# Kernel optimization log

Hardware: AMD Instinct MI355X
Metric: run time of the kernel (lower is better)

Reference implementation:

```python
import jax, jax.numpy as jnp
import numpy as np

N = 50000      # nodes
E = 800000     # edges (avg degree 16)
HID = 64       # hidden_dim
NH = 4         # heads
HC = HID // NH # channels per head = 16
EMB = 8        # emb_dim
EDIM = 6       # edge_dim
SDIM = 6       # state_dim
FEAT = 7       # raw node feature width
NSENS = 3


def setup_inputs() -> dict:
    key = jax.random.key(0)
    k = jax.random.split(key, 32)
    s = 0.1
    p = {}
    p['x'] = jax.random.normal(k[0], (N, FEAT), jnp.float32)
    p['node_type'] = jax.random.randint(k[1], (N,), 0, 2)
    p['sensor_id'] = jax.random.randint(k[2], (N,), 0, NSENS + 1)
    p['edge_index'] = jax.random.randint(k[3], (2, E), 0, N)
    p['edge_attr'] = jax.random.normal(k[4], (E, EDIM), jnp.float32)
    p['hidden_state'] = jnp.zeros((N, HID), jnp.float32)
    # embeddings
    p['type_emb'] = jax.random.normal(k[5], (2, EMB)) * s
    p['sensor_emb'] = jax.random.normal(k[6], (NSENS + 1, EMB)) * s
    # encoder MLP
    p['enc_w1'] = jax.random.normal(k[7], (FEAT + 2 * EMB, HID)) * s
    p['enc_b1'] = jnp.zeros((HID,))
    p['enc_w2'] = jax.random.normal(k[8], (HID, HID)) * s
    p['enc_b2'] = jnp.zeros((HID,))
    # GATv2 layer 1 (lin_l, lin_r with bias; lin_edge no bias; att [NH,HC]; out bias)
    p['g1_wl'] = jax.random.normal(k[9], (HID, HID)) * s
    p['g1_bl'] = jnp.zeros((HID,))
    p['g1_wr'] = jax.random.normal(k[10], (HID, HID)) * s
    p['g1_br'] = jnp.zeros((HID,))
    p['g1_we'] = jax.random.normal(k[11], (EDIM, HID)) * s
    p['g1_att'] = jax.random.normal(k[12], (NH, HC)) * s
    p['g1_bias'] = jnp.zeros((HID,))
    # GATv2 layer 2
    p['g2_wl'] = jax.random.normal(k[13], (HID, HID)) * s
    p['g2_bl'] = jnp.zeros((HID,))
    p['g2_wr'] = jax.random.normal(k[14], (HID, HID)) * s
    p['g2_br'] = jnp.zeros((HID,))
    p['g2_we'] = jax.random.normal(k[15], (EDIM, HID)) * s
    p['g2_att'] = jax.random.normal(k[16], (NH, HC)) * s
    p['g2_bias'] = jnp.zeros((HID,))
    # GRUCell (torch layout transposed: [in, 3*hid], gate order r,z,n)
    p['gru_wih'] = jax.random.normal(k[17], (HID, 3 * HID)) * s
    p['gru_bih'] = jnp.zeros((3 * HID,))
    p['gru_whh'] = jax.random.normal(k[18], (HID, 3 * HID)) * s
    p['gru_bhh'] = jnp.zeros((3 * HID,))
    # decoder MLP
    p['dec_w1'] = jax.random.normal(k[19], (HID, HID)) * s
    p['dec_b1'] = jnp.zeros((HID,))
    p['dec_w2'] = jax.random.normal(k[20], (HID, SDIM + 1)) * s
    p['dec_b2'] = jnp.zeros((SDIM + 1,))
    return p


def _gatv2(h, src, dst, edge_attr, wl, bl, wr, br, we, att, bias):
    # PyG GATv2Conv, concat=True, negative_slope=0.2, edge_dim features
    xl = (h @ wl + bl).reshape(-1, NH, HC)  # source transform [N,H,C]
    xr = (h @ wr + br).reshape(-1, NH, HC)  # target transform [N,H,C]
    xe = (edge_attr @ we).reshape(-1, NH, HC)  # edge transform [E,H,C]
    m = jax.nn.leaky_relu(xl[src] + xr[dst] + xe, 0.2)  # [E,H,C]
    logits = jnp.einsum('ehc,hc->eh', m, att)  # [E,H]
    # scatter-softmax over incoming edges of each destination node
    mx = jax.ops.segment_max(logits, dst, num_segments=N)
    ex = jnp.exp(logits - mx[dst])
    den = jax.ops.segment_sum(ex, dst, num_segments=N)
    alpha = ex / (den[dst] + 1e-16)  # [E,H]
    out = jax.ops.segment_sum(xl[src] * alpha[:, :, None], dst, num_segments=N)
    return out.reshape(-1, NH * HC) + bias, alpha


def reference(x, node_type, sensor_id, edge_index, edge_attr, hidden_state,
              type_emb, sensor_emb, enc_w1, enc_b1, enc_w2, enc_b2,
              g1_wl, g1_bl, g1_wr, g1_br, g1_we, g1_att, g1_bias,
              g2_wl, g2_bl, g2_wr, g2_br, g2_we, g2_att, g2_bias,
              gru_wih, gru_bih, gru_whh, gru_bhh,
              dec_w1, dec_b1, dec_w2, dec_b2):
    src, dst = edge_index[0], edge_index[1]
    h = jnp.concatenate([x, type_emb[node_type], sensor_emb[sensor_id]], axis=-1)
    h = jax.nn.relu(h @ enc_w1 + enc_b1) @ enc_w2 + enc_b2
    h, alpha1 = _gatv2(h, src, dst, edge_attr, g1_wl, g1_bl, g1_wr, g1_br, g1_we, g1_att, g1_bias)
    h = jax.nn.relu(h)
    h, alpha2 = _gatv2(h, src, dst, edge_attr, g2_wl, g2_bl, g2_wr, g2_br, g2_we, g2_att, g2_bias)
    # GRUCell (torch gate order: r, z, n)
    gi = h @ gru_wih + gru_bih
    gh = hidden_state @ gru_whh + gru_bhh
    r = jax.nn.sigmoid(gi[:, :HID] + gh[:, :HID])
    z = jax.nn.sigmoid(gi[:, HID:2 * HID] + gh[:, HID:2 * HID])
    n = jnp.tanh(gi[:, 2 * HID:] + r * gh[:, 2 * HID:])
    new_hidden = (1.0 - z) * n + z * hidden_state
    out = jax.nn.relu(new_hidden @ dec_w1 + dec_b1) @ dec_w2 + dec_b2
    return out, new_hidden, alpha1, alpha2
```

## Files before the change

kernel.cpp:

```cpp
#include <hip/hip_runtime.h>
#include <hip/hip_bf16.h>

static constexpr int N_ = 50000;
static constexpr int E_ = 800000;
static constexpr int CAP = 128;


#define GEMM_FMA_BLOCK(AV, W0, W1, ROW)                                              \
      acc[ROW][0]=fmaf(AV,W0.x,acc[ROW][0]); acc[ROW][1]=fmaf(AV,W0.y,acc[ROW][1]);  \
      acc[ROW][2]=fmaf(AV,W0.z,acc[ROW][2]); acc[ROW][3]=fmaf(AV,W0.w,acc[ROW][3]);  \
      acc[ROW][4]=fmaf(AV,W1.x,acc[ROW][4]); acc[ROW][5]=fmaf(AV,W1.y,acc[ROW][5]);  \
      acc[ROW][6]=fmaf(AV,W1.z,acc[ROW][6]); acc[ROW][7]=fmaf(AV,W1.w,acc[ROW][7]);

#define GEMM_KLOOP(KQc)                                                              \
  _Pragma("unroll 1")                                                                \
  for (int kg = 0; kg < (KQc); ++kg) {                                               \
    float4 a0 = At4[kg * 129 + rowb];                                                \
    float4 a1 = At4[kg * 129 + rowb + 32];                                           \
    float4 a2 = At4[kg * 129 + rowb + 64];                                           \
    float4 a3 = At4[kg * 129 + rowb + 96];                                           \
    _Pragma("unroll")                                                                \
    for (int t = 0; t < 4; ++t) {                                                    \
      float4 w0 = *(const float4*)(Wt + (kg * 4 + t) * 64 + j0);                     \
      float4 w1 = *(const float4*)(Wt + (kg * 4 + t) * 64 + j0 + 4);                 \
      float av0 = t==0?a0.x:t==1?a0.y:t==2?a0.z:a0.w;                                \
      float av1 = t==0?a1.x:t==1?a1.y:t==2?a1.z:a1.w;                                \
      float av2 = t==0?a2.x:t==1?a2.y:t==2?a2.z:a2.w;                                \
      float av3 = t==0?a3.x:t==1?a3.y:t==2?a3.z:a3.w;                                \
      GEMM_FMA_BLOCK(av0, w0, w1, 0)                                                 \
      GEMM_FMA_BLOCK(av1, w0, w1, 1)                                                 \
      GEMM_FMA_BLOCK(av2, w0, w1, 2)                                                 \
      GEMM_FMA_BLOCK(av3, w0, w1, 3)                                                 \
    }                                                                                \
  }

#define ACC_INIT(BPTR)                                                               \
  {                                                                                  \
    float4 b0v = *(const float4*)((BPTR) + j0);                                      \
    float4 b1v = *(const float4*)((BPTR) + j0 + 4);                                  \
    _Pragma("unroll")                                                                \
    for (int i = 0; i < 4; ++i) {                                                    \
      acc[i][0]=b0v.x; acc[i][1]=b0v.y; acc[i][2]=b0v.z; acc[i][3]=b0v.w;            \
      acc[i][4]=b1v.x; acc[i][5]=b1v.y; acc[i][6]=b1v.z; acc[i][7]=b1v.w;            \
    }                                                                                \
  }

#define STAGE_W(WPTR, LDW, KPADc, KREAL)                                             \
  for (int idx = tid; idx < (KPADc) * 16; idx += 256) {                              \
    int k = idx >> 4, jq = idx & 15;                                                 \
    float4 v = (k < (KREAL)) ? *(const float4*)((WPTR) + (size_t)k * (LDW) + jq * 4) \
                             : make_float4(0.f, 0.f, 0.f, 0.f);                      \
    *(float4*)(Wt + k * 64 + jq * 4) = v;                                            \
  }

#define STAGE_A(APTR, LDA, KQc)                                                      \
  for (int idx = tid; idx < 128 * (KQc); idx += 256) {                               \
    int r = idx / (KQc), kq = idx - r * (KQc);                                       \
    int node = nb + r;                                                               \
    float4 v = (node < N_) ? *(const float4*)((APTR) + (size_t)node * (LDA) + kq * 4)\
                           : make_float4(0.f, 0.f, 0.f, 0.f);                        \
    At4[kq * 129 + r] = v;                                                           \
  }

#define STORE_C(CPTR, LDC, RELUc, ACCc)                                              \
  _Pragma("unroll")                                                                  \
  for (int i = 0; i < 4; ++i) {                                                      \
    int node = nb + rowb + 32 * i;                                                   \
    if (node < N_) {                                                                 \
      float* cp = (CPTR) + (size_t)node * (LDC) + j0;                                \
      float o0=acc[i][0],o1=acc[i][1],o2=acc[i][2],o3=acc[i][3];                     \
      float o4=acc[i][4],o5=acc[i][5],o6=acc[i][6],o7=acc[i][7];                     \
      if (RELUc) { o0=fmaxf(o0,0.f);o1=fmaxf(o1,0.f);o2=fmaxf(o2,0.f);o3=fmaxf(o3,0.f); \
                   o4=fmaxf(o4,0.f);o5=fmaxf(o5,0.f);o6=fmaxf(o6,0.f);o7=fmaxf(o7,0.f); } \
      if (ACCc) { float4 c0=*(const float4*)cp; float4 c1=*(const float4*)(cp+4);    \
                  o0+=c0.x;o1+=c0.y;o2+=c0.z;o3+=c0.w;o4+=c1.x;o5+=c1.y;o6+=c1.z;o7+=c1.w; } \
      *(float4*)cp = make_float4(o0,o1,o2,o3);                                       \
      *(float4*)(cp+4) = make_float4(o4,o5,o6,o7);                                   \
    }                                                                                \
  }

__global__ void k_hist(const int* __restrict__ ei, int* __restrict__ deg) {
  int e = blockIdx.x * blockDim.x + threadIdx.x;
  if (e < E_) atomicAdd(&deg[ei[E_ + e]], 1);
}

__global__ __launch_bounds__(1024) void k_scan_blk(const int* __restrict__ deg,
                                                   int* __restrict__ off,
                                                   int* __restrict__ bsum) {
  __shared__ int sm[1024];
  int t = threadIdx.x;
  int i = blockIdx.x * 1024 + t;
  int v = (i < N_) ? deg[i] : 0;
  sm[t] = v;
  __syncthreads();
  for (int s = 1; s < 1024; s <<= 1) {
    int u = (t >= s) ? sm[t - s] : 0;
    __syncthreads();
    sm[t] += u;
    __syncthreads();
  }
  if (i < N_) off[i] = sm[t] - v;
  if (t == 1023) bsum[blockIdx.x] = sm[t];
}

__global__ void k_scan_top(int* __restrict__ bsum, int nb) {
  int t = threadIdx.x;
  int v = (t < nb) ? bsum[t] : 0;
  int orig = v;
  for (int s = 1; s < 64; s <<= 1) {
    int u = __shfl_up(v, s);
    if (t >= s) v += u;
  }
  if (t < nb) bsum[t] = v - orig;
}

__global__ void k_scan_add(int* __restrict__ off, const int* __restrict__ bsum,
                           int* __restrict__ cur) {
  int i = blockIdx.x * blockDim.x + threadIdx.x;
  if (i < N_) {
    int o = off[i] + bsum[i >> 10];
    off[i] = o;
    cur[i] = o;
  }
  if (i == 0) off[N_] = E_;
}

__global__ void k_scatter(const int* __restrict__ ei, int* __restrict__ cursor,
                          int2* __restrict__ csr_es) {
  int e = blockIdx.x * blockDim.x + threadIdx.x;
  if (e < E_) {
    int s = ei[e];
    int d = ei[E_ + e];
    int p = atomicAdd(&cursor[d], 1);
    csr_es[p] = make_int2(e, s);
  }
}

__device__ __forceinline__ float encval(int c, int node, int nt, int sd,
                                        const float* __restrict__ x,
                                        const float* __restrict__ temb,
                                        const float* __restrict__ semb) {
  if (c < 7) return x[node * 7 + c];
  if (c < 15) return temb[nt * 8 + c - 7];
  if (c < 23) return semb[sd * 8 + c - 15];
  return 0.f;
}

__global__ __launch_bounds__(256, 3) void k_enc(
    const float* __restrict__ x, const int* __restrict__ ntype, const int* __restrict__ sid,
    const float* __restrict__ temb, const float* __restrict__ semb,
    const float* __restrict__ w1, const float* __restrict__ b1,
    const float* __restrict__ w2, const float* __restrict__ b2,
    float* __restrict__ hout) {
  __shared__ float4 At4[16 * 129];
  __shared__ float Wt[64 * 64];
  int tid = threadIdx.x;
  int nb = blockIdx.x * 128;
  for (int idx = tid; idx < 128 * 6; idx += 256) {
    int r = idx / 6, kq = idx - r * 6;
    int node = nb + r;
    float v0 = 0.f, v1 = 0.f, v2 = 0.f, v3 = 0.f;
    if (node < N_) {
      int nt = ntype[node], sd = sid[node];
      int c = kq * 4;
      v0 = encval(c, node, nt, sd, x, temb, semb);
      v1 = encval(c + 1, node, nt, sd, x, temb, semb);
      v2 = encval(c + 2, node, nt, sd, x, temb, semb);
      v3 = encval(c + 3, node, nt, sd, x, temb, semb);
    }
    At4[kq * 129 + r] = make_float4(v0, v1, v2, v3);
  }
  STAGE_W(w1, 64, 24, 23)
  __syncthreads();
  int col = tid & 7, rowb = tid >> 3;
  int j0 = col * 8;
  float acc[4][8];
  ACC_INIT(b1)
  GEMM_KLOOP(6)
  __syncthreads();
#pragma unroll
  for (int i = 0; i < 4; ++i) {
    int rl = rowb + 32 * i;
    At4[(col * 2) * 129 + rl] =
        make_float4(fmaxf(acc[i][0], 0.f), fmaxf(acc[i][1], 0.f),
                    fmaxf(acc[i][2], 0.f), fmaxf(acc[i][3], 0.f));
    At4[(col * 2 + 1) * 129 + rl] =
        make_float4(fmaxf(acc[i][4], 0.f), fmaxf(acc[i][5], 0.f),
                    fmaxf(acc[i][6], 0.f), fmaxf(acc[i][7], 0.f));
  }
  STAGE_W(w2, 64, 64, 64)
  __syncthreads();
  ACC_INIT(b2)
  GEMM_KLOOP(16)
  STORE_C(hout, 64, false, false)
}

__global__ __launch_bounds__(256, 3) void k_gemm2(
    const float* __restrict__ A,
    const float* __restrict__ Wl, const float* __restrict__ bl,
    const float* __restrict__ Wr, const float* __restrict__ br,
    float* __restrict__ Cl, float* __restrict__ Cr) {
  __shared__ float4 At4[16 * 129];
  __shared__ float Wt[64 * 64];
  int tid = threadIdx.x;
  int nb = blockIdx.x * 128;
  const float* W = blockIdx.y ? Wr : Wl;
  const float* b = blockIdx.y ? br : bl;
  float* C       = blockIdx.y ? Cr : Cl;
  STAGE_A(A, 64, 16)
  STAGE_W(W, 64, 64, 64)
  __syncthreads();
  int col = tid & 7, rowb = tid >> 3;
  int j0 = col * 8;
  float acc[4][8];
  ACC_INIT(b)
  GEMM_KLOOP(16)
  STORE_C(C, 64, false, false)
}

__global__ __launch_bounds__(256, 3) void k_gru(
    const float* __restrict__ hA, const float* __restrict__ hs,
    const float* __restrict__ wih, const float* __restrict__ bih,
    const float* __restrict__ whh, const float* __restrict__ bhh,
    float* __restrict__ outnh) {
  __shared__ float4 At4[16 * 129];
  __shared__ float Wt[64 * 64];
  int tid = threadIdx.x;
  int nb = blockIdx.x * 128;
  int col = tid & 7, rowb = tid >> 3;
  int j0 = col * 8;
  float g0[4][8], g1[4][8], g2[4][8];
  STAGE_A(hA, 64, 16)
  STAGE_W(wih + 0, 192, 64, 64)
  __syncthreads();
  { auto& acc = g0; ACC_INIT(bih + 0) GEMM_KLOOP(16) }
  __syncthreads();
  STAGE_W(wih + 64, 192, 64, 64)
  __syncthreads();
  { auto& acc = g1; ACC_INIT(bih + 64) GEMM_KLOOP(16) }
  __syncthreads();
  STAGE_W(wih + 128, 192, 64, 64)
  __syncthreads();
  { auto& acc = g2; ACC_INIT(bih + 128) GEMM_KLOOP(16) }
  __syncthreads();
  STAGE_A(hs, 64, 16)
  STAGE_W(whh + 0, 192, 64, 64)
  __syncthreads();
  float gh[4][8];
  { auto& acc = gh; ACC_INIT(bhh + 0) GEMM_KLOOP(16) }
#pragma unroll
  for (int i = 0; i < 4; ++i)
#pragma unroll
    for (int u = 0; u < 8; ++u)
      g0[i][u] = 1.f / (1.f + __expf(-(g0[i][u] + gh[i][u])));
  __syncthreads();
  STAGE_W(whh + 64, 192, 64, 64)
  __syncthreads();
  { auto& acc = gh; ACC_INIT(bhh + 64) GEMM_KLOOP(16) }
#pragma unroll
  for (int i = 0; i < 4; ++i)
#pragma unroll
    for (int u = 0; u < 8; ++u)
      g1[i][u] = 1.f / (1.f + __expf(-(g1[i][u] + gh[i][u])));
  __syncthreads();
  STAGE_W(whh + 128, 192, 64, 64)
  __syncthreads();
  { auto& acc = gh; ACC_INIT(bhh + 128) GEMM_KLOOP(16) }
#pragma unroll
  for (int i = 0; i < 4; ++i)
#pragma unroll
    for (int u = 0; u < 8; ++u)
      g2[i][u] = tanhf(g2[i][u] + g0[i][u] * gh[i][u]);
#pragma unroll
  for (int i = 0; i < 4; ++i) {
    int node = nb + rowb + 32 * i;
    if (node < N_) {
      int rl = rowb + 32 * i;
      float4 s0 = At4[(col * 2) * 129 + rl];
      float4 s1 = At4[(col * 2 + 1) * 129 + rl];
      float q0 = (1.f - g1[i][0]) * g2[i][0] + g1[i][0] * s0.x;
      float q1 = (1.f - g1[i][1]) * g2[i][1] + g1[i][1] * s0.y;
      float q2 = (1.f - g1[i][2]) * g2[i][2] + g1[i][2] * s0.z;
      float q3 = (1.f - g1[i][3]) * g2[i][3] + g1[i][3] * s0.w;
      float q4 = (1.f - g1[i][4]) * g2[i][4] + g1[i][4] * s1.x;
      float q5 = (1.f - g1[i][5]) * g2[i][5] + g1[i][5] * s1.y;
      float q6 = (1.f - g1[i][6]) * g2[i][6] + g1[i][6] * s1.z;
      float q7 = (1.f - g1[i][7]) * g2[i][7] + g1[i][7] * s1.w;
      float* op = outnh + (size_t)node * 64 + j0;
      *(float4*)op = make_float4(q0, q1, q2, q3);
      *(float4*)(op + 4) = make_float4(q4, q5, q6, q7);
    }
  }
}

__global__ __launch_bounds__(256, 3) void k_dec(
    const float* __restrict__ A,
    const float* __restrict__ w1, const float* __restrict__ b1,
    const float* __restrict__ w2, const float* __restrict__ b2,
    float* __restrict__ out) {
  __shared__ __align__(16) float pool[8320];
  __shared__ float Wt[64 * 64];
  float4* At4 = (float4*)pool;
  float* dtile = pool;
  int tid = threadIdx.x;
  int nb = blockIdx.x * 128;
  STAGE_A(A, 64, 16)
  STAGE_W(w1, 64, 64, 64)
  __syncthreads();
  int col = tid & 7, rowb = tid >> 3;
  int j0 = col * 8;
  float acc[4][8];
  ACC_INIT(b1)
  GEMM_KLOOP(16)
  __syncthreads();
#pragma unroll
  for (int i = 0; i < 4; ++i) {
    int rl = rowb + 32 * i;
#pragma unroll
    for (int u = 0; u < 8; ++u) dtile[rl * 65 + j0 + u] = fmaxf(acc[i][u], 0.f);
  }
  __syncthreads();
  if (tid < 128) {
    int node = nb + tid;
    if (node < N_) {
      float o0 = b2[0], o1 = b2[1], o2 = b2[2], o3 = b2[3], o4 = b2[4], o5 = b2[5], o6 = b2[6];
#pragma unroll 1
      for (int k = 0; k < 64; ++k) {
        float xv = dtile[tid * 65 + k];
        o0 = fmaf(xv, w2[k * 7 + 0], o0);
        o1 = fmaf(xv, w2[k * 7 + 1], o1);
        o2 = fmaf(xv, w2[k * 7 + 2], o2);
        o3 = fmaf(xv, w2[k * 7 + 3], o3);
        o4 = fmaf(xv, w2[k * 7 + 4], o4);
        o5 = fmaf(xv, w2[k * 7 + 5], o5);
        o6 = fmaf(xv, w2[k * 7 + 6], o6);
      }
      float* op = out + (size_t)node * 7;
      op[0] = o0; op[1] = o1; op[2] = o2; op[3] = o3; op[4] = o4; op[5] = o5; op[6] = o6;
    }
  }
}

#define EDGE_STEP(XLS, EA, VALID, IDXBASE, EIDX)                                     \
  { float m0 = XLS.x + xr4.x, m1 = XLS.y + xr4.y;                                    \
    float m2 = XLS.z + xr4.z, m3 = XLS.w + xr4.w;                                    \
    _Pragma("unroll")                                                                \
    for (int i = 0; i < 6; ++i) {                                                    \
      float eai = __shfl(EA, sb + i);                                                \
      float4 w4 = *(const float4*)(wes + i * 64 + q * 4);                            \
      m0 = fmaf(eai, w4.x, m0); m1 = fmaf(eai, w4.y, m1);                            \
      m2 = fmaf(eai, w4.z, m2); m3 = fmaf(eai, w4.w, m3);                            \
    }                                                                                \
    m0 = (m0 > 0.f) ? m0 : 0.2f * m0;                                                \
    m1 = (m1 > 0.f) ? m1 : 0.2f * m1;                                                \
    m2 = (m2 > 0.f) ? m2 : 0.2f * m2;                                                \
    m3 = (m3 > 0.f) ? m3 : 0.2f * m3;                                                \
    float t = m0 * att4[0];                                                          \
    t = fmaf(m1, att4[1], t);                                                        \
    t = fmaf(m2, att4[2], t);                                                        \
    t = fmaf(m3, att4[3], t);                                                        \
    t += __shfl_xor(t, 1);                                                           \
    t += __shfl_xor(t, 2);                                                           \
    float ex = (VALID) ? __expf(t) : 0.f;                                            \
    den += ex;                                                                       \
    num0 = fmaf(XLS.x, ex, num0);                                                    \
    num1 = fmaf(XLS.y, ex, num1);                                                    \
    num2 = fmaf(XLS.z, ex, num2);                                                    \
    num3 = fmaf(XLS.w, ex, num3);                                                    \
    int idx = (IDXBASE) + slot;                                                      \
    if ((VALID) && idx < CAP) {                                                      \
      if ((lane & 3) == 0) exbuf[idx * 4 + head] = ex;                               \
      if (q == 0) ebuf[idx] = (EIDX);                                                \
    } }

template <bool RELU>
__global__ __launch_bounds__(64, 6) void k_fused(
    const int* __restrict__ off, const int2* __restrict__ csr_es,
    const float* __restrict__ eattr,
    const float* __restrict__ xl, const float* __restrict__ xr,
    const float* __restrict__ we, const float* __restrict__ att,
    const float* __restrict__ bias,
    float* __restrict__ hout, float* __restrict__ alpha) {
  __shared__ float wes[6 * 64];
  __shared__ float exbuf[CAP * 4];
  __shared__ int ebuf[CAP];
  int lane = threadIdx.x & 63;
  int slot = lane >> 4;
  int q = lane & 15;
  int head = q >> 2;
  int sb = slot << 4;
  int v = blockIdx.x;

#pragma unroll
  for (int i = 0; i < 6; ++i) wes[i * 64 + lane] = we[i * 64 + lane];

  int p0 = off[v], p1 = off[v + 1];
  int cnt = p1 - p0;

  float att4[4], b4[4];
#pragma unroll
  for (int r = 0; r < 4; ++r) { att4[r] = att[q * 4 + r]; b4[r] = bias[q * 4 + r]; }

  float4 xr4 = *(const float4*)(xr + (size_t)v * 64 + q * 4);
  float num0 = 0.f, num1 = 0.f, num2 = 0.f, num3 = 0.f, den = 0.f;

  __syncthreads();

  int2 esA = (p0 + slot < p1) ? csr_es[p0 + slot] : make_int2(0, 0);
  int2 esB = (p0 + 4 + slot < p1) ? csr_es[p0 + 4 + slot] : make_int2(0, 0);
  for (int base = 0; base < cnt; base += 8) {
    int pnA = p0 + base + 8 + slot;
    int pnB = p0 + base + 12 + slot;
    int2 esnA = (pnA < p1) ? csr_es[pnA] : make_int2(0, 0);
    int2 esnB = (pnB < p1) ? csr_es[pnB] : make_int2(0, 0);
    bool vA = (p0 + base + slot) < p1;
    bool vB = (p0 + base + 4 + slot) < p1;
    float eaA = (vA && q < 6) ? eattr[(size_t)esA.x * 6 + q] : 0.f;
    float eaB = (vB && q < 6) ? eattr[(size_t)esB.x * 6 + q] : 0.f;
    float4 xlsA = vA ? *(const float4*)(xl + (size_t)esA.y * 64 + q * 4)
                     : make_float4(0.f, 0.f, 0.f, 0.f);
    float4 xlsB = vB ? *(const float4*)(xl + (size_t)esB.y * 64 + q * 4)
                     : make_float4(0.f, 0.f, 0.f, 0.f);
    EDGE_STEP(xlsA, eaA, vA, base, esA.x)
    EDGE_STEP(xlsB, eaB, vB, base + 4, esB.x)
    esA = esnA; esB = esnB;
  }
  num0 += __shfl_xor(num0, 16); num0 += __shfl_xor(num0, 32);
  num1 += __shfl_xor(num1, 16); num1 += __shfl_xor(num1, 32);
  num2 += __shfl_xor(num2, 16); num2 += __shfl_xor(num2, 32);
  num3 += __shfl_xor(num3, 16); num3 += __shfl_xor(num3, 32);
  den  += __shfl_xor(den, 16);  den  += __shfl_xor(den, 32);
  float dinv = 1.f / (den + 1e-16f);
  float o0 = fmaf(num0, dinv, b4[0]);
  float o1 = fmaf(num1, dinv, b4[1]);
  float o2 = fmaf(num2, dinv, b4[2]);
  float o3 = fmaf(num3, dinv, b4[3]);
  if (RELU) {
    o0 = fmaxf(o0, 0.f); o1 = fmaxf(o1, 0.f); o2 = fmaxf(o2, 0.f); o3 = fmaxf(o3, 0.f);
  }
  if (slot == 0)
    *(float4*)(hout + (size_t)v * 64 + q * 4) = make_float4(o0, o1, o2, o3);
  float dh = __shfl(dinv, (lane & 3) << 2);
  if (cnt <= CAP) {
    for (int base2 = 0; base2 < cnt; base2 += 16) {
      int idx = base2 + (lane >> 2);
      if (idx < cnt) {
        float exv = exbuf[idx * 4 + (lane & 3)];
        int e = ebuf[idx];
        __builtin_nontemporal_store(exv * dh, &alpha[(size_t)e * 4 + (lane & 3)]);
      }
    }
  } else {
    for (int pp = p0; pp < p1; ++pp) {
      int2 es2 = csr_es[pp];
      int e = es2.x, s = es2.y;
      float ea = (q < 6) ? eattr[(size_t)e * 6 + q] : 0.f;
      float4 xls = *(const float4*)(xl + (size_t)s * 64 + q * 4);
      float m0 = xls.x + xr4.x, m1 = xls.y + xr4.y, m2 = xls.z + xr4.z, m3 = xls.w + xr4.w;
#pragma unroll
      for (int i = 0; i < 6; ++i) {
        float eai = __shfl(ea, i);
        float4 w4 = *(const float4*)(wes + i * 64 + q * 4);
        m0 = fmaf(eai, w4.x, m0);
        m1 = fmaf(eai, w4.y, m1);
        m2 = fmaf(eai, w4.z, m2);
        m3 = fmaf(eai, w4.w, m3);
      }
      m0 = (m0 > 0.f) ? m0 : 0.2f * m0;
      m1 = (m1 > 0.f) ? m1 : 0.2f * m1;
      m2 = (m2 > 0.f) ? m2 : 0.2f * m2;
      m3 = (m3 > 0.f) ? m3 : 0.2f * m3;
      float t = m0 * att4[0];
      t = fmaf(m1, att4[1], t);
      t = fmaf(m2, att4[2], t);
      t = fmaf(m3, att4[3], t);
      t += __shfl_xor(t, 1);
      t += __shfl_xor(t, 2);
      if (slot == 0 && (lane & 3) == 0)
        __builtin_nontemporal_store(__expf(t) * dinv, &alpha[(size_t)e * 4 + head]);
    }
  }
}

extern "C" void kernel_launch(void* const* d_in, const int* in_sizes, int n_in,
                              void* d_out, int out_size, void* d_ws, size_t ws_size,
                              hipStream_t stream) {
  const float* x      = (const float*)d_in[0];
  const int* ntype    = (const int*)d_in[1];
  const int* sid      = (const int*)d_in[2];
  const int* ei       = (const int*)d_in[3];
  const float* eattr  = (const float*)d_in[4];
  const float* hs     = (const float*)d_in[5];
  const float* temb   = (const float*)d_in[6];
  const float* semb   = (const float*)d_in[7];
  const float* enc_w1 = (const float*)d_in[8];
  const float* enc_b1 = (const float*)d_in[9];
  const float* enc_w2 = (const float*)d_in[10];
  const float* enc_b2 = (const float*)d_in[11];
  const float* g1_wl  = (const float*)d_in[12];
  const float* g1_bl  = (const float*)d_in[13];
  const float* g1_wr  = (const float*)d_in[14];
  const float* g1_br  = (const float*)d_in[15];
  const float* g1_we  = (const float*)d_in[16];
  const float* g1_att = (const float*)d_in[17];
  const float* g1_bias= (const float*)d_in[18];
  const float* g2_wl  = (const float*)d_in[19];
  const float* g2_bl  = (const float*)d_in[20];
  const float* g2_wr  = (const float*)d_in[21];
  const float* g2_br  = (const float*)d_in[22];
  const float* g2_we  = (const float*)d_in[23];
  const float* g2_att = (const float*)d_in[24];
  const float* g2_bias= (const float*)d_in[25];
  const float* gru_wih= (const float*)d_in[26];
  const float* gru_bih= (const float*)d_in[27];
  const float* gru_whh= (const float*)d_in[28];
  const float* gru_bhh= (const float*)d_in[29];
  const float* dec_w1 = (const float*)d_in[30];
  const float* dec_b1 = (const float*)d_in[31];
  const float* dec_w2 = (const float*)d_in[32];
  const float* dec_b2 = (const float*)d_in[33];

  float* ws = (float*)d_ws;
  float* hA = ws;
  float* hB = hA + N_ * 64;
  float* xl = hB + N_ * 64;
  float* xr = xl + N_ * 64;
  float* U  = xr + N_ * 64;
  int* deg  = (int*)(U + N_ * 64);
  int* off  = deg + N_;
  int* cur  = off + N_ + 1;
  int* bsum = cur + N_;
  int2* csr_es = (int2*)(bsum + 64);

  float* out0  = (float*)d_out;
  float* outnh = out0 + N_ * 7;
  float* outa1 = outnh + N_ * 64;
  float* outa2 = outa1 + E_ * 4;

  const int NB_SCAN = (N_ + 1023) / 1024;
  const int NB_GEMM = (N_ + 127) / 128;

  hipMemsetAsync(deg, 0, N_ * sizeof(int), stream);
  k_hist<<<(E_ + 255) / 256, 256, 0, stream>>>(ei, deg);
  k_scan_blk<<<NB_SCAN, 1024, 0, stream>>>(deg, off, bsum);
  k_scan_top<<<1, 64, 0, stream>>>(bsum, NB_SCAN);
  k_scan_add<<<(N_ + 255) / 256, 256, 0, stream>>>(off, bsum, cur);
  k_scatter<<<(E_ + 255) / 256, 256, 0, stream>>>(ei, cur, csr_es);

  k_enc<<<NB_GEMM, 256, 0, stream>>>(x, ntype, sid, temb, semb,
                                     enc_w1, enc_b1, enc_w2, enc_b2, hA);
  k_gemm2<<<dim3(NB_GEMM, 2), 256, 0, stream>>>(hA, g1_wl, g1_bl, g1_wr, g1_br, xl, xr);
  k_fused<true><<<N_, 64, 0, stream>>>(off, csr_es, eattr, xl, xr,
                                       g1_we, g1_att, g1_bias, hB, outa1);
  k_gemm2<<<dim3(NB_GEMM, 2), 256, 0, stream>>>(hB, g2_wl, g2_bl, g2_wr, g2_br, xl, xr);
  k_fused<false><<<N_, 64, 0, stream>>>(off, csr_es, eattr, xl, xr,
                                        g2_we, g2_att, g2_bias, hA, outa2);
  k_gru<<<NB_GEMM, 256, 0, stream>>>(hA, hs, gru_wih, gru_bih, gru_whh, gru_bhh, outnh);
  k_dec<<<NB_GEMM, 256, 0, stream>>>(outnh, dec_w1, dec_b1, dec_w2, dec_b2, out0);
}
```

Baseline: 579.1 us.

## Permute edge attributes into CSR order and simplify the edge loop

Adds a kernel that gathers edge attributes into destination-sorted CSR order as float4 and float2 arrays, so both GAT layers read them contiguously instead of gathering from random edge ids. The fused edge loop drops its two-edge unrolled prefetch and now handles one edge per slot per iteration, and the alpha writes switch from nontemporal to ordinary stores. The permutation costs an extra pass over the edge attributes and reuses the U workspace, and the smaller unroll may expose more memory latency in the edge loop.

```diff
diff --git a/kernel.cpp b/kernel.cpp
--- a/kernel.cpp
+++ b/kernel.cpp
@@ -133,6 +133,17 @@
     int d = ei[E_ + e];
     int p = atomicAdd(&cursor[d], 1);
     csr_es[p] = make_int2(e, s);
+  }
+}
+
+__global__ void k_eaperm(const int2* __restrict__ csr_es, const float* __restrict__ eattr,
+                         float4* __restrict__ eaA, float2* __restrict__ eaB) {
+  int p = blockIdx.x * blockDim.x + threadIdx.x;
+  if (p < E_) {
+    int e = csr_es[p].x;
+    const float* ep = eattr + (size_t)e * 6;
+    eaA[p] = make_float4(ep[0], ep[1], ep[2], ep[3]);
+    eaB[p] = make_float2(ep[4], ep[5]);
   }
 }
 
@@ -341,42 +352,10 @@
   }
 }
 
-#define EDGE_STEP(XLS, EA, VALID, IDXBASE, EIDX)                                     \
-  { float m0 = XLS.x + xr4.x, m1 = XLS.y + xr4.y;                                    \
-    float m2 = XLS.z + xr4.z, m3 = XLS.w + xr4.w;                                    \
-    _Pragma("unroll")                                                                \
-    for (int i = 0; i < 6; ++i) {                                                    \
-      float eai = __shfl(EA, sb + i);                                                \
-      float4 w4 = *(const float4*)(wes + i * 64 + q * 4);                            \
-      m0 = fmaf(eai, w4.x, m0); m1 = fmaf(eai, w4.y, m1);                            \
-      m2 = fmaf(eai, w4.z, m2); m3 = fmaf(eai, w4.w, m3);                            \
-    }                                                                                \
-    m0 = (m0 > 0.f) ? m0 : 0.2f * m0;                                                \
-    m1 = (m1 > 0.f) ? m1 : 0.2f * m1;                                                \
-    m2 = (m2 > 0.f) ? m2 : 0.2f * m2;                                                \
-    m3 = (m3 > 0.f) ? m3 : 0.2f * m3;                                                \
-    float t = m0 * att4[0];                                                          \
-    t = fmaf(m1, att4[1], t);                                                        \
-    t = fmaf(m2, att4[2], t);                                                        \
-    t = fmaf(m3, att4[3], t);                                                        \
-    t += __shfl_xor(t, 1);                                                           \
-    t += __shfl_xor(t, 2);                                                           \
-    float ex = (VALID) ? __expf(t) : 0.f;                                            \
-    den += ex;                                                                       \
-    num0 = fmaf(XLS.x, ex, num0);                                                    \
-    num1 = fmaf(XLS.y, ex, num1);                                                    \
-    num2 = fmaf(XLS.z, ex, num2);                                                    \
-    num3 = fmaf(XLS.w, ex, num3);                                                    \
-    int idx = (IDXBASE) + slot;                                                      \
-    if ((VALID) && idx < CAP) {                                                      \
-      if ((lane & 3) == 0) exbuf[idx * 4 + head] = ex;                               \
-      if (q == 0) ebuf[idx] = (EIDX);                                                \
-    } }
-
 template <bool RELU>
 __global__ __launch_bounds__(64, 6) void k_fused(
     const int* __restrict__ off, const int2* __restrict__ csr_es,
-    const float* __restrict__ eattr,
+    const float* __restrict__ eaA, const float* __restrict__ eaB,
     const float* __restrict__ xl, const float* __restrict__ xr,
     const float* __restrict__ we, const float* __restrict__ att,
     const float* __restrict__ bias,
@@ -406,24 +385,53 @@
 
   __syncthreads();
 
-  int2 esA = (p0 + slot < p1) ? csr_es[p0 + slot] : make_int2(0, 0);
-  int2 esB = (p0 + 4 + slot < p1) ? csr_es[p0 + 4 + slot] : make_int2(0, 0);
-  for (int base = 0; base < cnt; base += 8) {
-    int pnA = p0 + base + 8 + slot;
-    int pnB = p0 + base + 12 + slot;
-    int2 esnA = (pnA < p1) ? csr_es[pnA] : make_int2(0, 0);
-    int2 esnB = (pnB < p1) ? csr_es[pnB] : make_int2(0, 0);
-    bool vA = (p0 + base + slot) < p1;
-    bool vB = (p0 + base + 4 + slot) < p1;
-    float eaA = (vA && q < 6) ? eattr[(size_t)esA.x * 6 + q] : 0.f;
-    float eaB = (vB && q < 6) ? eattr[(size_t)esB.x * 6 + q] : 0.f;
-    float4 xlsA = vA ? *(const float4*)(xl + (size_t)esA.y * 64 + q * 4)
-                     : make_float4(0.f, 0.f, 0.f, 0.f);
-    float4 xlsB = vB ? *(const float4*)(xl + (size_t)esB.y * 64 + q * 4)
-                     : make_float4(0.f, 0.f, 0.f, 0.f);
-    EDGE_STEP(xlsA, eaA, vA, base, esA.x)
-    EDGE_STEP(xlsB, eaB, vB, base + 4, esB.x)
-    esA = esnA; esB = esnB;
+  int p = p0 + slot;
+  int2 es = (p < p1) ? csr_es[p] : make_int2(0, 0);
+  for (int base = 0; base < cnt; base += 4) {
+    int pc = p0 + base + slot;
+    bool valid = pc < p1;
+    int e = es.x, s = es.y;
+    int pn = pc + 4;
+    int2 esn = (pn < p1) ? csr_es[pn] : make_int2(0, 0);
+    float ea = 0.f;
+    if (valid) {
+      if (q < 4)      ea = eaA[(size_t)pc * 4 + q];
+      else if (q < 6) ea = eaB[(size_t)pc * 2 + (q - 4)];
+    }
+    float4 xls = valid ? *(const float4*)(xl + (size_t)s * 64 + q * 4)
+                       : make_float4(0.f, 0.f, 0.f, 0.f);
+    float m0 = xls.x + xr4.x, m1 = xls.y + xr4.y, m2 = xls.z + xr4.z, m3 = xls.w + xr4.w;
+#pragma unroll
+    for (int i = 0; i < 6; ++i) {
+      float eai = __shfl(ea, sb + i);
+      float4 w4 = *(const float4*)(wes + i * 64 + q * 4);
+      m0 = fmaf(eai, w4.x, m0);
+      m1 = fmaf(eai, w4.y, m1);
+      m2 = fmaf(eai, w4.z, m2);
+      m3 = fmaf(eai, w4.w, m3);
+    }
+    m0 = (m0 > 0.f) ? m0 : 0.2f * m0;
+    m1 = (m1 > 0.f) ? m1 : 0.2f * m1;
+    m2 = (m2 > 0.f) ? m2 : 0.2f * m2;
+    m3 = (m3 > 0.f) ? m3 : 0.2f * m3;
+    float t = m0 * att4[0];
+    t = fmaf(m1, att4[1], t);
+    t = fmaf(m2, att4[2], t);
+    t = fmaf(m3, att4[3], t);
+    t += __shfl_xor(t, 1);
+    t += __shfl_xor(t, 2);
+    float ex = valid ? __expf(t) : 0.f;
+    den += ex;
+    num0 = fmaf(xls.x, ex, num0);
+    num1 = fmaf(xls.y, ex, num1);
+    num2 = fmaf(xls.z, ex, num2);
+    num3 = fmaf(xls.w, ex, num3);
+    int idx = base + slot;
+    if (valid && idx < CAP) {
+      if ((lane & 3) == 0) exbuf[idx * 4 + head] = ex;
+      if (q == 0) ebuf[idx] = e;
+    }
+    es = esn;
   }
   num0 += __shfl_xor(num0, 16); num0 += __shfl_xor(num0, 32);
   num1 += __shfl_xor(num1, 16); num1 += __shfl_xor(num1, 32);
@@ -447,14 +455,16 @@
       if (idx < cnt) {
         float exv = exbuf[idx * 4 + (lane & 3)];
         int e = ebuf[idx];
-        __builtin_nontemporal_store(exv * dh, &alpha[(size_t)e * 4 + (lane & 3)]);
+        alpha[(size_t)e * 4 + (lane & 3)] = exv * dh;
       }
     }
   } else {
     for (int pp = p0; pp < p1; ++pp) {
       int2 es2 = csr_es[pp];
       int e = es2.x, s = es2.y;
-      float ea = (q < 6) ? eattr[(size_t)e * 6 + q] : 0.f;
+      float ea = 0.f;
+      if (q < 4)      ea = eaA[(size_t)pp * 4 + q];
+      else if (q < 6) ea = eaB[(size_t)pp * 2 + (q - 4)];
       float4 xls = *(const float4*)(xl + (size_t)s * 64 + q * 4);
       float m0 = xls.x + xr4.x, m1 = xls.y + xr4.y, m2 = xls.z + xr4.z, m3 = xls.w + xr4.w;
 #pragma unroll
@@ -477,7 +487,7 @@
       t += __shfl_xor(t, 1);
       t += __shfl_xor(t, 2);
       if (slot == 0 && (lane & 3) == 0)
-        __builtin_nontemporal_store(__expf(t) * dinv, &alpha[(size_t)e * 4 + head]);
+        alpha[(size_t)e * 4 + head] = __expf(t) * dinv;
     }
   }
 }
@@ -531,6 +541,9 @@
   int* cur  = off + N_ + 1;
   int* bsum = cur + N_;
   int2* csr_es = (int2*)(bsum + 64);
+  float2* eaB = (float2*)(csr_es + E_);
+
+  float4* eaA = (float4*)U;
 
   float* out0  = (float*)d_out;
   float* outnh = out0 + N_ * 7;
@@ -546,15 +559,16 @@
   k_scan_top<<<1, 64, 0, stream>>>(bsum, NB_SCAN);
   k_scan_add<<<(N_ + 255) / 256, 256, 0, stream>>>(off, bsum, cur);
   k_scatter<<<(E_ + 255) / 256, 256, 0, stream>>>(ei, cur, csr_es);
+  k_eaperm<<<(E_ + 255) / 256, 256, 0, stream>>>(csr_es, eattr, eaA, eaB);
 
   k_enc<<<NB_GEMM, 256, 0, stream>>>(x, ntype, sid, temb, semb,
                                      enc_w1, enc_b1, enc_w2, enc_b2, hA);
   k_gemm2<<<dim3(NB_GEMM, 2), 256, 0, stream>>>(hA, g1_wl, g1_bl, g1_wr, g1_br, xl, xr);
-  k_fused<true><<<N_, 64, 0, stream>>>(off, csr_es, eattr, xl, xr,
-                                       g1_we, g1_att, g1_bias, hB, outa1);
+  k_fused<true><<<N_, 64, 0, stream>>>(off, csr_es, (const float*)eaA, (const float*)eaB,
+                                       xl, xr, g1_we, g1_att, g1_bias, hB, outa1);
   k_gemm2<<<dim3(NB_GEMM, 2), 256, 0, stream>>>(hB, g2_wl, g2_bl, g2_wr, g2_br, xl, xr);
-  k_fused<false><<<N_, 64, 0, stream>>>(off, csr_es, eattr, xl, xr,
-                                        g2_we, g2_att, g2_bias, hA, outa2);
+  k_fused<false><<<N_, 64, 0, stream>>>(off, csr_es, (const float*)eaA, (const float*)eaB,
+                                        xl, xr, g2_we, g2_att, g2_bias, hA, outa2);
   k_gru<<<NB_GEMM, 256, 0, stream>>>(hA, hs, gru_wih, gru_bih, gru_whh, gru_bhh, outnh);
   k_dec<<<NB_GEMM, 256, 0, stream>>>(outnh, dec_w1, dec_b1, dec_w2, dec_b2, out0);
 }
```

Measured after the change: 521.5 us. 1.11x faster.
